# Performance work log

Hardware: AMD Instinct MI355X
Metric: run time of the kernel (lower is better)

## Reference

```python
import jax, jax.numpy as jnp
import numpy as np

B = 4096          # batch_size
D_EMB = 16        # per-side embedding dim (embed_to_from width = 2*D_EMB)
D_HIGH = 784      # flattened high-dim feature size
NSR = 5           # negative_sample_rate
A = 1.576943      # UMAP _a
B_PARAM = 0.8950608  # UMAP _b
REPULSION = 1.0
EPS = 1e-4
GLOBAL_LOSS = 0.5
TOTAL_STEPS = 1000
BATCH_COUNT = 500  # fixed step for deterministic alpha/beta
WARMUP = int(0.05 * TOTAL_STEPS)


def _safe_sqrt(sq):
    # sqrt with zero (not NaN) gradient at 0, matching zero-distance pairs
    safe = jnp.where(sq > 0, sq, 1.0)
    return jnp.where(sq > 0, jnp.sqrt(safe), 0.0)


def _pairwise_dist(x):
    # ||x_i - x_j|| via gram trick; avoids materializing [N,N,D]
    sq = jnp.sum(x * x, axis=1)                      # [N]
    gram = x @ x.T                                   # [N,N]
    d2 = sq[:, None] + sq[None, :] - 2.0 * gram
    return _safe_sqrt(jnp.maximum(d2, 0.0))


def _umap_ce_loss(embed_to_from, perm):
    e_to, e_from = jnp.split(embed_to_from, 2, axis=1)   # [B, D_EMB] each
    neg_to = jnp.repeat(e_to, NSR, axis=0)               # [B*NSR, D_EMB]
    repeat_neg = jnp.repeat(e_from, NSR, axis=0)
    neg_from = repeat_neg[perm]                          # shuffled negatives
    d_pos = _safe_sqrt(jnp.sum((e_to - e_from) ** 2, axis=1))
    d_neg = _safe_sqrt(jnp.sum((neg_to - neg_from) ** 2, axis=1))
    dist = jnp.concatenate([d_pos, d_neg], axis=0)       # [B*(1+NSR)]
    p_dist = 1.0 / (1.0 + A * dist ** (2.0 * B_PARAM))
    p_graph = jnp.concatenate([jnp.ones(B, p_dist.dtype), jnp.zeros(B * NSR, p_dist.dtype)])
    attraction = -p_graph * jnp.log(jnp.clip(p_dist, EPS, 1.0))
    repellant = -(1.0 - p_graph) * jnp.log(jnp.clip(1.0 - p_dist, EPS, 1.0)) * REPULSION
    return jnp.mean(attraction + repellant)


def _global_feature_loss(embed_to_from, to_x):
    e_to = embed_to_from[:, :D_EMB]
    to_x = to_x.reshape(to_x.shape[0], -1)
    high_dis = _pairwise_dist(to_x)     # [N,N]
    low_dis = _pairwise_dist(e_to)      # [N,N]
    # row-wise pearson correlation between high_dis and low_dis
    h = high_dis - jnp.mean(high_dis, axis=1, keepdims=True)
    l = low_dis - jnp.mean(low_dis, axis=1, keepdims=True)
    num = jnp.sum(h * l, axis=1)
    den = jnp.sqrt(jnp.sum(h * h, axis=1)) * jnp.sqrt(jnp.sum(l * l, axis=1))
    corr = jnp.mean(num / den)
    return -corr


def _alpha_beta():
    if BATCH_COUNT >= WARMUP:
        if BATCH_COUNT <= 0.9 * TOTAL_STEPS:
            beta = max(0.0, GLOBAL_LOSS * (1 - BATCH_COUNT / (TOTAL_STEPS - WARMUP * 4)) ** 2)
        else:
            beta = 0.0
        alpha = max(0.0, 1 - beta)
    else:
        alpha = 0.0
        beta = GLOBAL_LOSS
    return alpha, beta


def setup_inputs() -> dict:
    key = jax.random.key(0)
    k1, k2, k3 = jax.random.split(key, 3)
    embed_to_from = jax.random.normal(k1, (B, 2 * D_EMB), dtype=jnp.float32)
    placeholder = jax.random.normal(k2, (B, D_HIGH), dtype=jnp.float32)
    perm = jax.random.permutation(k3, B * NSR).astype(jnp.int32)
    return {"embed_to_from": embed_to_from, "placeholder": placeholder, "perm": perm}


def reference(embed_to_from, placeholder, perm):
    loss = _umap_ce_loss(embed_to_from, perm)
    loss_g = _global_feature_loss(embed_to_from, placeholder)
    alpha, beta = _alpha_beta()
    return alpha * loss + beta * loss_g
```

## Files before the change

### kernel.cpp

```cpp
#include <hip/hip_runtime.h>
#include <hip/hip_bf16.h>
#include <math.h>

#define NB    4096
#define DH    784
#define KX8   832
#define NSR   5
#define NNEG  (NB*NSR)
#define NTOT  (NB + NNEG)

#define A_CONST 1.576943f
#define PEXP    1.7901216f
#define EPS_C   1.0e-4f
#define ALPHA_C 0.9296875f
#define BETA_C  0.0703125f

#define NSLOT 64
#define SLAB  (NB * NSLOT)
#define NBLK  528
#define BUFB  8192

typedef __hip_bfloat16 bf16;
typedef short bf16x8 __attribute__((ext_vector_type(8)));
typedef float f32x4  __attribute__((ext_vector_type(4)));
typedef float f32x2  __attribute__((ext_vector_type(2)));
typedef long long2v __attribute__((ext_vector_type(2)));

#define WS_XF8    0
#define WS_EBF    3407872
#define WS_SQX    3670016
#define WS_SQE    3686400
#define WS_STATSP 3702784
#define WS_UPART  8945664
#define WS_CPART  8946048
#define WS_CNT    8946304

__device__ __forceinline__ void gl2lds16(const void* g, void* l) {
    __builtin_amdgcn_global_load_lds(
        (const __attribute__((address_space(1))) unsigned int*)g,
        (__attribute__((address_space(3))) unsigned int*)l,
        16, 0, 0);
}

__global__ void prep_fused(const float* __restrict__ X, const float* __restrict__ emb,
                           const int* __restrict__ perm, unsigned char* __restrict__ Xf8,
                           float* __restrict__ sqx, bf16* __restrict__ Ebf,
                           float* __restrict__ sqe, float* __restrict__ upart,
                           unsigned* __restrict__ cnt) {
    if (blockIdx.x == 0 && threadIdx.x == 0) *cnt = 0u;
    if (blockIdx.x < 1024) {
        const int wave = threadIdx.x >> 6, lane = threadIdx.x & 63;
        const int row = blockIdx.x * 4 + wave;
        const float4* xr = (const float4*)(X + (size_t)row * DH);
        int* xb = (int*)(Xf8 + (size_t)row * KX8);
        float s = 0.f;
        #pragma unroll
        for (int it = 0; it < 4; ++it) {
            const int idx = lane + it * 64;
            if (idx < 208) {
                const int c = idx >> 4, p = idx & 15;
                const int q = p >> 2, h = (p >> 1) & 1, w = p & 1;
                const int src = c * 16 + h * 8 + q * 2 + w;
                int pk = 0;
                if (src < 196) {
                    float4 v = xr[src];
                    s += v.x * v.x + v.y * v.y + v.z * v.z + v.w * v.w;
                    int lo = __builtin_amdgcn_cvt_pk_fp8_f32(v.x, v.y, 0, false);
                    pk = __builtin_amdgcn_cvt_pk_fp8_f32(v.z, v.w, lo, true);
                }
                xb[idx] = pk;
            }
        }
        #pragma unroll
        for (int off = 32; off; off >>= 1) s += __shfl_down(s, off, 64);
        if (lane == 0) sqx[row] = s;
        return;
    }
    const int ub = blockIdx.x - 1024;
    const int t = ub * 256 + threadIdx.x;
    float val = 0.f;
    if (t < NB) {
        const float4* av = (const float4*)(emb + (size_t)t * 32);
        float4 t0 = av[0], t1 = av[1], t2 = av[2], t3 = av[3];
        float4 f0 = av[4], f1 = av[5], f2 = av[6], f3 = av[7];
        bf16* eb = Ebf + (size_t)t * 32;
        union { bf16 h[4]; ushort4 u; } cv;
        #define ST4(dst, q) cv.h[0]=__float2bfloat16(q.x); cv.h[1]=__float2bfloat16(q.y); \
                            cv.h[2]=__float2bfloat16(q.z); cv.h[3]=__float2bfloat16(q.w); \
                            *(ushort4*)(dst) = cv.u;
        ST4(eb,      t0) ST4(eb + 4,  t1) ST4(eb + 8,  t2) ST4(eb + 12, t3)
        #undef ST4
        ushort4 z = {0, 0, 0, 0};
        *(ushort4*)(eb + 16) = z; *(ushort4*)(eb + 20) = z;
        *(ushort4*)(eb + 24) = z; *(ushort4*)(eb + 28) = z;
        sqe[t] = t0.x*t0.x + t0.y*t0.y + t0.z*t0.z + t0.w*t0.w
               + t1.x*t1.x + t1.y*t1.y + t1.z*t1.z + t1.w*t1.w
               + t2.x*t2.x + t2.y*t2.y + t2.z*t2.z + t2.w*t2.w
               + t3.x*t3.x + t3.y*t3.y + t3.z*t3.z + t3.w*t3.w;
        float d2 = 0.f;
        #define D2(a, b) { float4 df = {a.x-b.x, a.y-b.y, a.z-b.z, a.w-b.w}; \
                           d2 += df.x*df.x + df.y*df.y + df.z*df.z + df.w*df.w; }
        D2(t0, f0) D2(t1, f1) D2(t2, f2) D2(t3, f3)
        #undef D2
        float d = sqrtf(d2);
        float p = 1.f / (1.f + A_CONST * powf(d, PEXP));
        val = -logf(fminf(fmaxf(p, EPS_C), 1.f));
    } else if (t < NTOT) {
        const int k = t - NB;
        const int ti = k / 5;
        const int fi = perm[k] / 5;
        const float4* at = (const float4*)(emb + (size_t)ti * 32);
        const float4* bt = (const float4*)(emb + (size_t)fi * 32 + 16);
        float d2 = 0.f;
        #pragma unroll
        for (int q = 0; q < 4; ++q) {
            float4 a = at[q], b = bt[q];
            float4 df = {a.x-b.x, a.y-b.y, a.z-b.z, a.w-b.w};
            d2 += df.x*df.x + df.y*df.y + df.z*df.z + df.w*df.w;
        }
        float d = sqrtf(d2);
        float p = 1.f / (1.f + A_CONST * powf(d, PEXP));
        val = -logf(fminf(fmaxf(1.f - p, EPS_C), 1.f));
    }
    #pragma unroll
    for (int off = 32; off; off >>= 1) val += __shfl_down(val, off, 64);
    __shared__ float ps[4];
    if ((threadIdx.x & 63) == 0) ps[threadIdx.x >> 6] = val;
    __syncthreads();
    if (threadIdx.x == 0) upart[ub] = ps[0] + ps[1] + ps[2] + ps[3];
}

__global__ __launch_bounds__(512, 4) void gram_kernel(
    const unsigned char* __restrict__ Xf8, const bf16* __restrict__ Ebf,
    const float* __restrict__ sqx, const float* __restrict__ sqe,
    float* __restrict__ statsp) {
    __shared__ __align__(16) unsigned char smem[51200];
    unsigned char* As = smem;
    unsigned char* Bs = smem + 3 * BUFB;
    float* sqxs = (float*)(smem + 49152);
    float* sqes = (float*)(smem + 50176);
    float* scr  = (float*)smem;

    int n = (blockIdx.x & 7) * 66 + (blockIdx.x >> 3);
    int bi = 0;
    while (n >= 32 - bi) { n -= 32 - bi; ++bi; }
    const int bj = bi + n;
    const int i0 = bi * 128, j0 = bj * 128;

    const int tid  = threadIdx.x;
    const int wave = tid >> 6;
    const int lane = tid & 63;
    const int wy = wave >> 1, wx = wave & 1;
    const int quad = lane >> 4, l15 = lane & 15;

    f32x4 acc[2][4];
    #pragma unroll
    for (int a = 0; a < 2; ++a)
        #pragma unroll
        for (int b = 0; b < 4; ++b)
            acc[a][b] = (f32x4){0.f, 0.f, 0.f, 0.f};

    const int rA  = lane >> 2;
    const int gsb = (((lane & 3) ^ ((lane >> 3) & 3))) * 16;
    const unsigned char* gA = Xf8 + (size_t)(i0 + wave * 16 + rA) * KX8 + gsb;
    const unsigned char* gB = Xf8 + (size_t)(j0 + wave * 16 + rA) * KX8 + gsb;

    if (tid < 128) {
        sqxs[tid] = sqx[i0 + tid]; sqxs[128 + tid] = sqx[j0 + tid];
        sqes[tid] = sqe[i0 + tid]; sqes[128 + tid] = sqe[j0 + tid];
    }
    __syncthreads();

    #pragma unroll
    for (int s = 0; s < 2; ++s) {
        gl2lds16(gA, As + s * BUFB + wave * 1024);
        gl2lds16(gB, Bs + s * BUFB + wave * 1024);
        gA += 64; gB += 64;
    }

    const int key = (l15 >> 1) & 3;
    const int boX = ((quad ^ key) << 4);

    int cur = 0;
    for (int t = 0; t < 13; ++t) {
        asm volatile("s_waitcnt vmcnt(2)" ::: "memory");
        __builtin_amdgcn_s_barrier();
        const int nb = (cur + 2 * BUFB >= 3 * BUFB) ? cur - BUFB : cur + 2 * BUFB;
        if (t < 11) {
            gl2lds16(gA, As + nb + wave * 1024);
            gl2lds16(gB, Bs + nb + wave * 1024);
            gA += 64; gB += 64;
        } else if (t == 11) {
            gl2lds16((const unsigned char*)(Ebf + (size_t)(i0 + wave * 16 + rA) * 32) + gsb,
                     As + BUFB + wave * 1024);
            gl2lds16((const unsigned char*)(Ebf + (size_t)(j0 + wave * 16 + rA) * 32) + gsb,
                     Bs + BUFB + wave * 1024);
        }
        long2v aF[2], bF[4];
        #pragma unroll
        for (int mi = 0; mi < 2; ++mi)
            aF[mi] = *(const long2v*)&As[cur + (wy * 32 + mi * 16 + l15) * 64 + boX];
        #pragma unroll
        for (int ni = 0; ni < 4; ++ni)
            bF[ni] = *(const long2v*)&Bs[cur + (wx * 64 + ni * 16 + l15) * 64 + boX];
        #pragma unroll
        for (int mi = 0; mi < 2; ++mi)
            #pragma unroll
            for (int ni = 0; ni < 4; ++ni) {
                acc[mi][ni] = __builtin_amdgcn_mfma_f32_16x16x32_fp8_fp8(
                    aF[mi][0], bF[ni][0], acc[mi][ni], 0, 0, 0);
                acc[mi][ni] = __builtin_amdgcn_mfma_f32_16x16x32_fp8_fp8(
                    aF[mi][1], bF[ni][1], acc[mi][ni], 0, 0, 0);
            }
        cur = (cur == 2 * BUFB) ? 0 : cur + BUFB;
    }
    asm volatile("s_waitcnt vmcnt(0)" ::: "memory");
    __builtin_amdgcn_s_barrier();

    bf16x8 afE[2], bfrE[4];
    #pragma unroll
    for (int mi = 0; mi < 2; ++mi)
        afE[mi] = *(const bf16x8*)&As[BUFB + (wy * 32 + mi * 16 + l15) * 64 + boX];
    #pragma unroll
    for (int ni = 0; ni < 4; ++ni)
        bfrE[ni] = *(const bf16x8*)&Bs[BUFB + (wx * 64 + ni * 16 + l15) * 64 + boX];
    float sqxj[4], sqej[4];
    #pragma unroll
    for (int ni = 0; ni < 4; ++ni) {
        const int jl = wx * 64 + ni * 16 + l15;
        sqxj[ni] = sqxs[128 + jl]; sqej[ni] = sqes[128 + jl];
    }
    __syncthreads();

    float cst[4][5];
    #pragma unroll
    for (int ni = 0; ni < 4; ++ni)
        #pragma unroll
        for (int c = 0; c < 5; ++c) cst[ni][c] = 0.f;

    #pragma unroll
    for (int mi = 0; mi < 2; ++mi) {
        f32x4 aE[4];
        #pragma unroll
        for (int ni = 0; ni < 4; ++ni) {
            f32x4 z = (f32x4){0.f, 0.f, 0.f, 0.f};
            aE[ni] = __builtin_amdgcn_mfma_f32_16x16x32_bf16(afE[mi], bfrE[ni], z, 0, 0, 0);
        }
        const int ilb = wy * 32 + mi * 16 + quad * 4;
        float sqxi[4], sqei[4];
        #pragma unroll
        for (int r = 0; r < 4; ++r) { sqxi[r] = sqxs[ilb + r]; sqei[r] = sqes[ilb + r]; }
        float rs[5][4];
        #pragma unroll
        for (int c = 0; c < 5; ++c)
            #pragma unroll
            for (int r = 0; r < 4; ++r) rs[c][r] = 0.f;
        #pragma unroll
        for (int ni = 0; ni < 4; ++ni) {
            const int j = j0 + wx * 64 + ni * 16 + l15;
            #pragma unroll
            for (int r = 0; r < 4; ++r) {
                const int i = i0 + ilb + r;
                float H, L;
                if (i == j) { H = 0.f; L = 0.f; }
                else {
                    float d2  = sqxi[r] + sqxj[ni] - 2.0f * acc[mi][ni][r];
                    H = sqrtf(fmaxf(d2, 0.f));
                    float d2e = sqei[r] + sqej[ni] - 2.0f * aE[ni][r];
                    L = sqrtf(fmaxf(d2e, 0.f));
                }
                rs[0][r] += H; rs[1][r] += H * H; rs[2][r] += L;
                rs[3][r] += L * L; rs[4][r] += H * L;
                cst[ni][0] += H; cst[ni][1] += H * H; cst[ni][2] += L;
                cst[ni][3] += L * L; cst[ni][4] += H * L;
            }
        }
        #pragma unroll
        for (int c = 0; c < 5; ++c)
            #pragma unroll
            for (int r = 0; r < 4; ++r)
                scr[(size_t)((((wx * 5 + c) << 6) + (wy << 4) + (quad << 2) + r)) * 18 + l15]
                    = rs[c][r];
        __syncthreads();
        for (int o = tid; o < 640; o += 512) {
            const int wxo = (o >= 320) ? 1 : 0;
            const int rem = o - wxo * 320;
            const int c = rem >> 6, li = rem & 63;
            const float* p = scr + (size_t)(((wxo * 5 + c) << 6) + li) * 18;
            float s = 0.f;
            #pragma unroll
            for (int k = 0; k < 16; k += 2) { f32x2 v = *(const f32x2*)&p[k]; s += v.x + v.y; }
            const int iloc = ((li >> 4) << 5) + mi * 16 + (li & 15);
            statsp[(size_t)c * SLAB + (size_t)(bj * 2 + wxo) * NB + (i0 + iloc)] = s;
        }
        __syncthreads();
    }

    if (bi != bj) {
        #pragma unroll
        for (int ni = 0; ni < 4; ++ni) {
            const int jl = wx * 64 + ni * 16 + l15;
            #pragma unroll
            for (int c = 0; c < 5; ++c)
                scr[(size_t)(c * 128 + jl) * 17 + (wy << 2) + quad] = cst[ni][c];
        }
        __syncthreads();
        for (int o = tid; o < 1280; o += 512) {
            const int c = o >> 8, h = (o >> 7) & 1, j = o & 127;
            const float* p = scr + (size_t)(c * 128 + j) * 17 + h * 8;
            float s = ((p[0] + p[1]) + (p[2] + p[3])) + ((p[4] + p[5]) + (p[6] + p[7]));
            statsp[(size_t)c * SLAB + (size_t)(bi * 2 + h) * NB + (j0 + j)] = s;
        }
    }
}

__global__ void finish1_kernel(const float* __restrict__ statsp, const float* __restrict__ upart,
                               float* __restrict__ cpart, unsigned* __restrict__ cnt,
                               float* __restrict__ out) {
    __shared__ float ps2[4][64][5];
    const int t = threadIdx.x;
    const int rloc = t & 63;
    const int sg = t >> 6;
    const int r = blockIdx.x * 64 + rloc;
    float sh = 0.f, sh2 = 0.f, sl = 0.f, sl2 = 0.f, shl = 0.f;
    for (int s = sg * 16; s < sg * 16 + 16; ++s) {
        const float* base = statsp + (size_t)s * NB + r;
        sh  += base[0 * SLAB];
        sh2 += base[1 * SLAB];
        sl  += base[2 * SLAB];
        sl2 += base[3 * SLAB];
        shl += base[4 * SLAB];
    }
    ps2[sg][rloc][0] = sh; ps2[sg][rloc][1] = sh2; ps2[sg][rloc][2] = sl;
    ps2[sg][rloc][3] = sl2; ps2[sg][rloc][4] = shl;
    __syncthreads();
    if (t < 64) {
        float a = 0.f, b = 0.f, c = 0.f, d = 0.f, e = 0.f;
        #pragma unroll
        for (int g = 0; g < 4; ++g) {
            a += ps2[g][t][0]; b += ps2[g][t][1]; c += ps2[g][t][2];
            d += ps2[g][t][3]; e += ps2[g][t][4];
        }
        const float invN = 1.0f / (float)NB;
        float num = e - a * c * invN;
        float vh  = fmaxf(b - a * a * invN, 0.f);
        float vl  = fmaxf(d - c * c * invN, 0.f);
        float local = num / (sqrtf(vh) * sqrtf(vl));
        #pragma unroll
        for (int off = 32; off; off >>= 1) local += __shfl_down(local, off, 64);
        if (t == 0) cpart[blockIdx.x] = local;
    }
    __shared__ int lastFlag;
    if (t == 0) {
        __threadfence();
        unsigned prev = atomicAdd(cnt, 1u);
        lastFlag = (prev == 63u);
    }
    __syncthreads();
    if (lastFlag) {
        __threadfence();
        float v = 0.f;
        if (t < 64) v += cpart[t] * (-BETA_C / (float)NB);
        if (t < 96) v += upart[t] * (ALPHA_C / (float)NTOT);
        #pragma unroll
        for (int off = 32; off; off >>= 1) v += __shfl_down(v, off, 64);
        __shared__ float fin[4];
        if ((t & 63) == 0) fin[t >> 6] = v;
        __syncthreads();
        if (t == 0) out[0] = fin[0] + fin[1] + fin[2] + fin[3];
    }
}

extern "C" void kernel_launch(void* const* d_in, const int* in_sizes, int n_in,
                              void* d_out, int out_size, void* d_ws, size_t ws_size,
                              hipStream_t stream) {
    const float* emb  = (const float*)d_in[0];
    const float* ph   = (const float*)d_in[1];
    const int*   perm = (const int*)d_in[2];
    float* out = (float*)d_out;

    char* ws = (char*)d_ws;
    unsigned char* Xf8 = (unsigned char*)(ws + WS_XF8);
    bf16*  Ebf    = (bf16*) (ws + WS_EBF);
    float* sqx    = (float*)(ws + WS_SQX);
    float* sqe    = (float*)(ws + WS_SQE);
    float* statsp = (float*)(ws + WS_STATSP);
    float* upart  = (float*)(ws + WS_UPART);
    float* cpart  = (float*)(ws + WS_CPART);
    unsigned* cnt = (unsigned*)(ws + WS_CNT);

    prep_fused<<<1120, 256, 0, stream>>>(ph, emb, perm, Xf8, sqx, Ebf, sqe, upart, cnt);
    gram_kernel<<<NBLK, 512, 0, stream>>>(Xf8, Ebf, sqx, sqe, statsp);
    finish1_kernel<<<64, 256, 0, stream>>>(statsp, upart, cpart, cnt, out);
}
```

Measured before the change: 121.2 us.

## Load gram MFMA fragments directly from global memory instead of LDS staging

The gram kernel no longer stages FP8 X tiles and bf16 embedding tiles through a triple-buffered LDS pipeline with global_load_lds and barriers. Each wave now loads its MFMA operand fragments straight from global memory into registers, using register double-buffering across K steps. This removes LDS traffic and per-step barriers and shrinks shared memory. In exchange, each wave re-fetches operand data that other waves in the block share, so more requests go through L1/L2, and load latency is hidden only by the two-deep register pipeline.

```diff
diff --git a/kernel.cpp b/kernel.cpp
--- a/kernel.cpp
+++ b/kernel.cpp
@@ -18,7 +18,6 @@
 #define NSLOT 64
 #define SLAB  (NB * NSLOT)
 #define NBLK  528
-#define BUFB  8192
 
 typedef __hip_bfloat16 bf16;
 typedef short bf16x8 __attribute__((ext_vector_type(8)));
@@ -34,13 +33,6 @@
 #define WS_UPART  8945664
 #define WS_CPART  8946048
 #define WS_CNT    8946304
-
-__device__ __forceinline__ void gl2lds16(const void* g, void* l) {
-    __builtin_amdgcn_global_load_lds(
-        (const __attribute__((address_space(1))) unsigned int*)g,
-        (__attribute__((address_space(3))) unsigned int*)l,
-        16, 0, 0);
-}
 
 __global__ void prep_fused(const float* __restrict__ X, const float* __restrict__ emb,
                            const int* __restrict__ perm, unsigned char* __restrict__ Xf8,
@@ -134,12 +126,10 @@
     const unsigned char* __restrict__ Xf8, const bf16* __restrict__ Ebf,
     const float* __restrict__ sqx, const float* __restrict__ sqe,
     float* __restrict__ statsp) {
-    __shared__ __align__(16) unsigned char smem[51200];
-    unsigned char* As = smem;
-    unsigned char* Bs = smem + 3 * BUFB;
-    float* sqxs = (float*)(smem + 49152);
-    float* sqes = (float*)(smem + 50176);
+    __shared__ __align__(16) unsigned char smem[48128];
     float* scr  = (float*)smem;
+    float* sqxs = (float*)(smem + 46080);
+    float* sqes = (float*)(smem + 47104);
 
     int n = (blockIdx.x & 7) * 66 + (blockIdx.x >> 3);
     int bi = 0;
@@ -160,77 +150,62 @@
         for (int b = 0; b < 4; ++b)
             acc[a][b] = (f32x4){0.f, 0.f, 0.f, 0.f};
 
-    const int rA  = lane >> 2;
-    const int gsb = (((lane & 3) ^ ((lane >> 3) & 3))) * 16;
-    const unsigned char* gA = Xf8 + (size_t)(i0 + wave * 16 + rA) * KX8 + gsb;
-    const unsigned char* gB = Xf8 + (size_t)(j0 + wave * 16 + rA) * KX8 + gsb;
-
     if (tid < 128) {
         sqxs[tid] = sqx[i0 + tid]; sqxs[128 + tid] = sqx[j0 + tid];
         sqes[tid] = sqe[i0 + tid]; sqes[128 + tid] = sqe[j0 + tid];
     }
     __syncthreads();
 
-    #pragma unroll
-    for (int s = 0; s < 2; ++s) {
-        gl2lds16(gA, As + s * BUFB + wave * 1024);
-        gl2lds16(gB, Bs + s * BUFB + wave * 1024);
-        gA += 64; gB += 64;
-    }
-
-    const int key = (l15 >> 1) & 3;
-    const int boX = ((quad ^ key) << 4);
-
-    int cur = 0;
-    for (int t = 0; t < 13; ++t) {
-        asm volatile("s_waitcnt vmcnt(2)" ::: "memory");
-        __builtin_amdgcn_s_barrier();
-        const int nb = (cur + 2 * BUFB >= 3 * BUFB) ? cur - BUFB : cur + 2 * BUFB;
-        if (t < 11) {
-            gl2lds16(gA, As + nb + wave * 1024);
-            gl2lds16(gB, Bs + nb + wave * 1024);
-            gA += 64; gB += 64;
-        } else if (t == 11) {
-            gl2lds16((const unsigned char*)(Ebf + (size_t)(i0 + wave * 16 + rA) * 32) + gsb,
-                     As + BUFB + wave * 1024);
-            gl2lds16((const unsigned char*)(Ebf + (size_t)(j0 + wave * 16 + rA) * 32) + gsb,
-                     Bs + BUFB + wave * 1024);
-        }
-        long2v aF[2], bF[4];
-        #pragma unroll
-        for (int mi = 0; mi < 2; ++mi)
-            aF[mi] = *(const long2v*)&As[cur + (wy * 32 + mi * 16 + l15) * 64 + boX];
-        #pragma unroll
-        for (int ni = 0; ni < 4; ++ni)
-            bF[ni] = *(const long2v*)&Bs[cur + (wx * 64 + ni * 16 + l15) * 64 + boX];
-        #pragma unroll
-        for (int mi = 0; mi < 2; ++mi)
-            #pragma unroll
-            for (int ni = 0; ni < 4; ++ni) {
-                acc[mi][ni] = __builtin_amdgcn_mfma_f32_16x16x32_fp8_fp8(
-                    aF[mi][0], bF[ni][0], acc[mi][ni], 0, 0, 0);
-                acc[mi][ni] = __builtin_amdgcn_mfma_f32_16x16x32_fp8_fp8(
-                    aF[mi][1], bF[ni][1], acc[mi][ni], 0, 0, 0);
-            }
-        cur = (cur == 2 * BUFB) ? 0 : cur + BUFB;
-    }
-    asm volatile("s_waitcnt vmcnt(0)" ::: "memory");
-    __builtin_amdgcn_s_barrier();
-
+    const unsigned char* pA = Xf8 + (size_t)(i0 + wy * 32 + l15) * KX8 + quad * 16;
+    const unsigned char* pB = Xf8 + (size_t)(j0 + wx * 64 + l15) * KX8 + quad * 16;
+
+    long2v aF0[2], bF0[4], aF1[2], bF1[4];
+#define LOADX(aF, bF, t) { \
+        aF[0] = *(const long2v*)(pA + (t) * 64); \
+        aF[1] = *(const long2v*)(pA + 16 * KX8 + (t) * 64); \
+        bF[0] = *(const long2v*)(pB + (t) * 64); \
+        bF[1] = *(const long2v*)(pB + 16 * KX8 + (t) * 64); \
+        bF[2] = *(const long2v*)(pB + 32 * KX8 + (t) * 64); \
+        bF[3] = *(const long2v*)(pB + 48 * KX8 + (t) * 64); }
+#define MMX(aF, bF) { \
+        _Pragma("unroll") \
+        for (int mi = 0; mi < 2; ++mi) { \
+            _Pragma("unroll") \
+            for (int ni = 0; ni < 4; ++ni) { \
+                acc[mi][ni] = __builtin_amdgcn_mfma_f32_16x16x32_fp8_fp8( \
+                    aF[mi][0], bF[ni][0], acc[mi][ni], 0, 0, 0); \
+                acc[mi][ni] = __builtin_amdgcn_mfma_f32_16x16x32_fp8_fp8( \
+                    aF[mi][1], bF[ni][1], acc[mi][ni], 0, 0, 0); \
+            } \
+        } }
+
+    LOADX(aF0, bF0, 0);
+    #pragma unroll
+    for (int t = 0; t < 12; t += 2) {
+        LOADX(aF1, bF1, t + 1);
+        MMX(aF0, bF0);
+        LOADX(aF0, bF0, t + 2);
+        MMX(aF1, bF1);
+    }
+    MMX(aF0, bF0);
+
+    const unsigned char* pAe = (const unsigned char*)Ebf
+                             + (size_t)(i0 + wy * 32 + l15) * 64 + quad * 16;
+    const unsigned char* pBe = (const unsigned char*)Ebf
+                             + (size_t)(j0 + wx * 64 + l15) * 64 + quad * 16;
     bf16x8 afE[2], bfrE[4];
     #pragma unroll
     for (int mi = 0; mi < 2; ++mi)
-        afE[mi] = *(const bf16x8*)&As[BUFB + (wy * 32 + mi * 16 + l15) * 64 + boX];
+        afE[mi] = *(const bf16x8*)(pAe + mi * 16 * 64);
     #pragma unroll
     for (int ni = 0; ni < 4; ++ni)
-        bfrE[ni] = *(const bf16x8*)&Bs[BUFB + (wx * 64 + ni * 16 + l15) * 64 + boX];
+        bfrE[ni] = *(const bf16x8*)(pBe + ni * 16 * 64);
     float sqxj[4], sqej[4];
     #pragma unroll
     for (int ni = 0; ni < 4; ++ni) {
         const int jl = wx * 64 + ni * 16 + l15;
         sqxj[ni] = sqxs[128 + jl]; sqej[ni] = sqes[128 + jl];
     }
-    __syncthreads();
 
     float cst[4][5];
     #pragma unroll
@@ -312,6 +287,8 @@
             statsp[(size_t)c * SLAB + (size_t)(bi * 2 + h) * NB + (j0 + j)] = s;
         }
     }
+#undef LOADX
+#undef MMX
 }
 
 __global__ void finish1_kernel(const float* __restrict__ statsp, const float* __restrict__ upart,
```

After: 135.3 us. 11.6% more time.
